# Kernel optimization log

Hardware: AMD Instinct MI355X
Metric: run time of the kernel (lower is better)

## Reference

```python
import jax, jax.numpy as jnp
import numpy as np
from functools import partial

B, T, F = 2048, 128, 64
H1, H2 = 512, 512


def _lstm(x, W, U, b, return_sequences):
    """Keras-semantics LSTM: gates order (i, f, c, o), recurrent_activation=sigmoid,
    cell activation=relu (as in activation='relu'). x: [B, T, F_in]."""
    Bs = x.shape[0]
    H = U.shape[0]
    # Precompute input contributions for all timesteps: [T, B, 4H]
    xg = (jnp.einsum('btf,fg->btg', x, W) + b).transpose(1, 0, 2)

    def step(carry, xt):
        h, c = carry
        g = xt + h @ U  # [B, 4H]
        i, f, cin, o = jnp.split(g, 4, axis=-1)
        i = jax.nn.sigmoid(i)
        f = jax.nn.sigmoid(f)
        o = jax.nn.sigmoid(o)
        c = f * c + i * jax.nn.relu(cin)
        h = o * jax.nn.relu(c)
        return (h, c), h

    h0 = jnp.zeros((Bs, H), dtype=x.dtype)
    c0 = jnp.zeros((Bs, H), dtype=x.dtype)
    (h, c), hs = jax.lax.scan(step, (h0, c0), xg)
    if return_sequences:
        return hs.transpose(1, 0, 2)  # [B, T, H]
    return h  # [B, H]


def setup_inputs() -> dict:
    key = jax.random.key(0)
    ks = jax.random.split(key, 9)
    s = 0.02  # small init so the relu cell stays numerically tame
    return {
        'x':  jax.random.normal(ks[0], (B, T, F), dtype=jnp.float32),
        'W1': jax.random.normal(ks[1], (F, 4 * H1), dtype=jnp.float32) * s,
        'U1': jax.random.normal(ks[2], (H1, 4 * H1), dtype=jnp.float32) * s,
        'b1': jnp.zeros((4 * H1,), dtype=jnp.float32),
        'W2': jax.random.normal(ks[3], (H1, 4 * H2), dtype=jnp.float32) * s,
        'U2': jax.random.normal(ks[4], (H2, 4 * H2), dtype=jnp.float32) * s,
        'b2': jnp.zeros((4 * H2,), dtype=jnp.float32),
        'Wd': jax.random.normal(ks[5], (H2, 1), dtype=jnp.float32) * s,
        'bd': jnp.zeros((1,), dtype=jnp.float32),
    }


def reference(x, W1, U1, b1, W2, U2, b2, Wd, bd):
    h1 = _lstm(x, W1, U1, b1, return_sequences=True)   # [B, T, H1]
    h2 = _lstm(h1, W2, U2, b2, return_sequences=False)  # [B, H2]
    return h2 @ Wd + bd  # [B, 1]
```

## Files before the change

### kernel.cpp

```cpp
#include <hip/hip_runtime.h>

#define TT   128
#define FF   64
#define HH   512
#define GG   2048
#define K1   576
#define K2   1024
#define KB1  72
#define KB2  128
#define NBLK 256
#define QS   520

using f16x8 = __attribute__((ext_vector_type(8))) _Float16;
using f16x4 = __attribute__((ext_vector_type(4))) _Float16;
using f32x4 = __attribute__((ext_vector_type(4))) float;

__global__ void pack_weights(const float* __restrict__ U, const float* __restrict__ W,
                             const float* __restrict__ bias, int K8, int Kh,
                             _Float16* __restrict__ Bp, float* __restrict__ pb)
{
    __shared__ _Float16 T[8][GG];
    const int kb = blockIdx.x;
    const int tid = threadIdx.x;
    for (int i = tid; i < 8 * (GG / 4); i += 256) {
        int r = i / (GG / 4), c4 = (i % (GG / 4)) * 4;
        int k = kb * 8 + r;
        const float* src = (k < Kh) ? (U + (size_t)k * GG) : (W + (size_t)(k - Kh) * GG);
        float4 v = *(const float4*)(src + c4);
        T[r][c4 + 0] = (_Float16)v.x; T[r][c4 + 1] = (_Float16)v.y;
        T[r][c4 + 2] = (_Float16)v.z; T[r][c4 + 3] = (_Float16)v.w;
    }
    __syncthreads();
    for (int m = tid; m < 2048; m += 256) {
        int ct = m >> 4, c = m & 15;
        int col = (c & 3) * HH + ct * 4 + (c >> 2);
        f16x8 v;
#pragma unroll
        for (int j = 0; j < 8; ++j) v[j] = T[j][col];
        *(f16x8*)(Bp + (((size_t)ct * K8 + kb) * 16 + c) * 8) = v;
    }
    if (kb == 0)
        for (int p = tid; p < GG; p += 256) {
            int ct = p >> 4, c = p & 15;
            pb[p] = bias[(c & 3) * HH + ct * 4 + (c >> 2)];
        }
}

template <int CTRL>
__device__ __forceinline__ float qbcast(float v) {
    return __int_as_float(__builtin_amdgcn_mov_dpp(__float_as_int(v), CTRL, 0xF, 0xF, true));
}

__device__ __forceinline__ void gld_lds16_sc0(const _Float16* g, _Float16* l) {
    __builtin_amdgcn_global_load_lds(
        (__attribute__((address_space(1))) const void*)g,
        (__attribute__((address_space(3))) void*)l, 16, 0, 1);
}

__device__ __forceinline__ void lstm_epi(
    f32x4 v4, float bias, float* __restrict__ cs, _Float16* __restrict__ hstp,
    int R0, int kq, int c, int ubase)
{
    const int gsel = c & 3;
    const int ub = ubase + (c >> 2);
#pragma unroll
    for (int j = 0; j < 4; ++j) {
        float v = v4[j] + bias;
        float sig = 1.f / (1.f + __expf(-v));
        float act = (gsel == 2) ? (v > 0.f ? v : 0.f) : sig;
        float ig  = qbcast<0x00>(act);
        float fg  = qbcast<0x55>(act);
        float cin = qbcast<0xAA>(act);
        float og  = qbcast<0xFF>(act);
        int Rl = kq * 4 + j;
        int R = R0 + Rl;
        float cp = cs[R * 33 + ub];
        float cn = fg * cp + ig * cin;
        float hn = og * (cn > 0.f ? cn : 0.f);
        if (gsel == 0) {
            cs[R * 33 + ub] = cn;
            hstp[Rl * 40 + ub] = (_Float16)hn;
        }
    }
}

#define MFMA16(av, bv, acc) \
    acc = __builtin_amdgcn_mfma_f32_16x16x32_f16(av, bv, acc, 0, 0, 0)

__global__ __launch_bounds__(256, 1) void lstm_persist(
    const float* __restrict__ x,
    const _Float16* __restrict__ Bp1, const float* __restrict__ pb1,
    const _Float16* __restrict__ Bp2, const float* __restrict__ pb2,
    const float* __restrict__ Wd, const float* __restrict__ bd,
    _Float16* __restrict__ h1b,
    _Float16* __restrict__ h2b,
    unsigned* __restrict__ bar,
    float* __restrict__ out)
{
    __shared__ _Float16 Q1[2][16 * QS];
    __shared__ _Float16 Q2[2][16 * QS];
    __shared__ _Float16 Xp[2][16][72];
    __shared__ float    c1s[128 * 33];
    __shared__ float    c2s[128 * 33];
    __shared__ _Float16 hst[2][2][16][40];
    __shared__ float    xb[2][2][2][2][2][256];

    const int tid = threadIdx.x;
    const int w = tid >> 6, lane = tid & 63;
    const int g = w >> 1, kh = w & 1;
    const int b = blockIdx.x;
    const int rg = 2 * (b & 7) + ((b >> 3) & 1);
    const int cg = b >> 4;
    const int r0 = rg * 128;
    const int c = lane & 15, kq = lane >> 4;

    for (int i = tid; i < 128 * 33; i += 256) { c1s[i] = 0.f; c2s[i] = 0.f; }

    f16x8 w1f[4][9], w2f[4][16];
#pragma unroll
    for (int ti = 0; ti < 4; ++ti) {
        const int ct = cg * 8 + g * 4 + ti;
#pragma unroll
        for (int kc = 0; kc < 9; ++kc)
            w1f[ti][kc] = *(const f16x8*)(Bp1 +
                (((size_t)ct * KB1 + (kh * 9 + kc) * 4 + kq) * 16 + c) * 8);
#pragma unroll
        for (int kc = 0; kc < 16; ++kc)
            w2f[ti][kc] = *(const f16x8*)(Bp2 +
                (((size_t)ct * KB2 + (kh * 16 + kc) * 4 + kq) * 16 + c) * 8);
    }
#pragma unroll
    for (int ti = 0; ti < 4; ++ti) {
#pragma unroll
        for (int kc = 0; kc < 9; ++kc) asm volatile("" : "+v"(w1f[ti][kc]));
#pragma unroll
        for (int kc = 0; kc < 16; ++kc) asm volatile("" : "+a"(w2f[ti][kc]));
    }

    const int ct0 = cg * 8 + g * 4 + kh * 2;
    const float bias1v[2] = { pb1[(ct0 + 0) * 16 + c], pb1[(ct0 + 1) * 16 + c] };
    const float bias2v[2] = { pb2[(ct0 + 0) * 16 + c], pb2[(ct0 + 1) * 16 + c] };
    const int ub0 = (g * 4 + kh * 2) * 4;

    const int xrow = tid >> 4, xc4 = (tid & 15) * 4;

    for (int s = 0; s <= TT; ++s) {
        const int pr1 = (s + 1) & 1, pw1 = s & 1;
        const int pr2 = s & 1,       pw2 = (s + 1) & 1;
        const _Float16* h1r = h1b + (size_t)pr1 * 2048 * HH;
        const _Float16* h2r = h2b + (size_t)pr2 * 2048 * HH;
        _Float16* h1w = h1b + (size_t)pw1 * 2048 * HH;
        _Float16* h2w = h2b + (size_t)pw2 * 2048 * HH;
        const bool notLast = (s < TT);

        {
#pragma unroll
            for (int i = 0; i < 4; ++i) {
                int r = w * 4 + i;
                gld_lds16_sc0(h1r + (size_t)(r0 + r) * HH + lane * 8, &Q1[0][r * QS]);
                gld_lds16_sc0(h2r + (size_t)(r0 + r) * HH + lane * 8, &Q2[0][r * QS]);
            }
            if (notLast) {
                float4 xv = *(const float4*)(x + ((size_t)(r0 + xrow) * TT + s) * FF + xc4);
                *(f16x4*)&Xp[0][xrow][xc4] =
                    (f16x4){(_Float16)xv.x, (_Float16)xv.y, (_Float16)xv.z, (_Float16)xv.w};
            }
        }
        __syncthreads();

        f32x4 ownA0{0.f, 0.f, 0.f, 0.f}, ownA1 = ownA0, ownB0 = ownA0, ownB1 = ownA0;

        for (int ch = 0; ch <= 9; ++ch) {
            const int par = ch & 1;

            if (ch <= 6) {
                const int gr = r0 + (ch + 1) * 16;
#pragma unroll
                for (int i = 0; i < 4; ++i) {
                    int r = w * 4 + i;
                    gld_lds16_sc0(h1r + (size_t)(gr + r) * HH + lane * 8, &Q1[par ^ 1][r * QS]);
                    gld_lds16_sc0(h2r + (size_t)(gr + r) * HH + lane * 8, &Q2[par ^ 1][r * QS]);
                }
            }
            float4 xnext{0.f, 0.f, 0.f, 0.f};
            const bool havex = (ch <= 6) && notLast;
            if (havex)
                xnext = *(const float4*)(x +
                    ((size_t)(r0 + (ch + 1) * 16 + xrow) * TT + s) * FF + xc4);

            if (ch >= 2) {
                int layer = tid >> 7, r = (tid >> 3) & 15, cq = tid & 7;
                bool go2 = layer ? (s >= 1) : notLast;
                if (go2) {
                    f16x4 hv = *(const f16x4*)&hst[par][layer][r][cq * 4];
                    _Float16* dst = (layer ? h2w : h1w)
                        + (size_t)(r0 + (ch - 2) * 16 + r) * HH + cg * 32 + cq * 4;
                    *(f16x4*)dst = hv;
                }
            }

            if (ch >= 1 && ch <= 8) {
                const int R0 = (ch - 1) * 16;
                if (notLast) {
                    f32x4 f0 = ownA0 + *(const f32x4*)&xb[par ^ 1][0][g][kh ^ 1][0][lane * 4];
                    f32x4 f1 = ownA1 + *(const f32x4*)&xb[par ^ 1][0][g][kh ^ 1][1][lane * 4];
                    lstm_epi(f0, bias1v[0], c1s, &hst[par ^ 1][0][0][0], R0, kq, c, ub0);
                    lstm_epi(f1, bias1v[1], c1s, &hst[par ^ 1][0][0][0], R0, kq, c, ub0 + 4);
                }
                if (s >= 1) {
                    f32x4 f0 = ownB0 + *(const f32x4*)&xb[par ^ 1][1][g][kh ^ 1][0][lane * 4];
                    f32x4 f1 = ownB1 + *(const f32x4*)&xb[par ^ 1][1][g][kh ^ 1][1][lane * 4];
                    lstm_epi(f0, bias2v[0], c2s, &hst[par ^ 1][1][0][0], R0, kq, c, ub0);
                    lstm_epi(f1, bias2v[1], c2s, &hst[par ^ 1][1][0][0], R0, kq, c, ub0 + 4);
                }
            }

            if (ch <= 7) {
                const char* q1b = (const char*)&Q1[par][0] + c * (QS * 2);
                const char* q2b = (const char*)&Q2[par][0] + c * (QS * 2);
                if (notLast) {
                    f32x4 a0{0.f, 0.f, 0.f, 0.f}, a1 = a0, a2 = a0, a3 = a0;
                    if (kh == 0) {
#pragma unroll
                        for (int kc = 0; kc < 9; ++kc) {
                            f16x8 av = *(const f16x8*)(q1b + kc * 64 + kq * 16);
                            MFMA16(av, w1f[0][kc], a0); MFMA16(av, w1f[1][kc], a1);
                            MFMA16(av, w1f[2][kc], a2); MFMA16(av, w1f[3][kc], a3);
                        }
                        *(f32x4*)&xb[par][0][g][0][0][lane * 4] = a2;
                        *(f32x4*)&xb[par][0][g][0][1][lane * 4] = a3;
                        ownA0 = a0; ownA1 = a1;
                    } else {
#pragma unroll
                        for (int kc = 0; kc < 7; ++kc) {
                            f16x8 av = *(const f16x8*)(q1b + (kc + 9) * 64 + kq * 16);
                            MFMA16(av, w1f[0][kc], a0); MFMA16(av, w1f[1][kc], a1);
                            MFMA16(av, w1f[2][kc], a2); MFMA16(av, w1f[3][kc], a3);
                        }
                        {
                            f16x8 av = *(const f16x8*)&Xp[par][c][kq * 8];
                            MFMA16(av, w1f[0][7], a0); MFMA16(av, w1f[1][7], a1);
                            MFMA16(av, w1f[2][7], a2); MFMA16(av, w1f[3][7], a3);
                        }
                        {
                            f16x8 av = *(const f16x8*)&Xp[par][c][32 + kq * 8];
                            MFMA16(av, w1f[0][8], a0); MFMA16(av, w1f[1][8], a1);
                            MFMA16(av, w1f[2][8], a2); MFMA16(av, w1f[3][8], a3);
                        }
                        *(f32x4*)&xb[par][0][g][1][0][lane * 4] = a0;
                        *(f32x4*)&xb[par][0][g][1][1][lane * 4] = a1;
                        ownA0 = a2; ownA1 = a3;
                    }
                }
                if (s >= 1) {
                    const char* qb = kh ? q1b : q2b;
                    f32x4 b0{0.f, 0.f, 0.f, 0.f}, b1 = b0, b2 = b0, b3 = b0;
#pragma unroll
                    for (int kc = 0; kc < 16; ++kc) {
                        f16x8 av = *(const f16x8*)(qb + kc * 64 + kq * 16);
                        MFMA16(av, w2f[0][kc], b0); MFMA16(av, w2f[1][kc], b1);
                        MFMA16(av, w2f[2][kc], b2); MFMA16(av, w2f[3][kc], b3);
                    }
                    if (kh == 0) {
                        *(f32x4*)&xb[par][1][g][0][0][lane * 4] = b2;
                        *(f32x4*)&xb[par][1][g][0][1][lane * 4] = b3;
                        ownB0 = b0; ownB1 = b1;
                    } else {
                        *(f32x4*)&xb[par][1][g][1][0][lane * 4] = b0;
                        *(f32x4*)&xb[par][1][g][1][1][lane * 4] = b1;
                        ownB0 = b2; ownB1 = b3;
                    }
                }
            }

            if (havex)
                *(f16x4*)&Xp[par ^ 1][xrow][xc4] =
                    (f16x4){(_Float16)xnext.x, (_Float16)xnext.y,
                            (_Float16)xnext.z, (_Float16)xnext.w};

            __syncthreads();
        }

        if (tid == 0) {
            __hip_atomic_fetch_add(&bar[rg * 32], 1u,
                                   __ATOMIC_RELAXED, __HIP_MEMORY_SCOPE_AGENT);
            const unsigned target = 16u * (unsigned)(s + 1);
            while (__hip_atomic_load(&bar[rg * 32],
                                     __ATOMIC_RELAXED, __HIP_MEMORY_SCOPE_AGENT) < target)
                __builtin_amdgcn_s_sleep(2);
        }
        __syncthreads();
    }

    if (cg == 0) {
        const _Float16* hf = h2b + (size_t)((TT + 1) & 1) * 2048 * HH;
        int row = tid >> 1, part = tid & 1;
        const _Float16* hr = hf + (size_t)(r0 + row) * HH + part * 256;
        const float* wd = Wd + part * 256;
        float ssum = 0.f;
#pragma unroll
        for (int u8 = 0; u8 < 32; ++u8) {
            f16x8 hv = *(const f16x8*)(hr + u8 * 8);
#pragma unroll
            for (int k = 0; k < 8; ++k) ssum += (float)hv[k] * wd[u8 * 8 + k];
        }
        ssum += __shfl_xor(ssum, 1);
        if (part == 0) out[r0 + row] = ssum + bd[0];
    }
}

extern "C" void kernel_launch(void* const* d_in, const int* in_sizes, int n_in,
                              void* d_out, int out_size, void* d_ws, size_t ws_size,
                              hipStream_t stream)
{
    const float* x  = (const float*)d_in[0];
    const float* W1 = (const float*)d_in[1];
    const float* U1 = (const float*)d_in[2];
    const float* b1 = (const float*)d_in[3];
    const float* W2 = (const float*)d_in[4];
    const float* U2 = (const float*)d_in[5];
    const float* b2 = (const float*)d_in[6];
    const float* Wd = (const float*)d_in[7];
    const float* bd = (const float*)d_in[8];
    float* out = (float*)d_out;

    char* ws = (char*)d_ws;
    size_t off = 0;
    _Float16* Bp1 = (_Float16*)(ws + off); off += (size_t)K1 * GG * 2;
    _Float16* Bp2 = (_Float16*)(ws + off); off += (size_t)K2 * GG * 2;
    float*    pb1 = (float*)(ws + off);    off += (size_t)GG * 4;
    float*    pb2 = (float*)(ws + off);    off += (size_t)GG * 4;
    _Float16* h1b = (_Float16*)(ws + off); off += (size_t)2 * 2048 * HH * 2;
    _Float16* h2b = (_Float16*)(ws + off); off += (size_t)2 * 2048 * HH * 2;
    unsigned* bar = (unsigned*)(ws + off); off += 16 * 32 * 4;

    hipMemsetAsync(h1b, 0, (size_t)2 * 2048 * HH * 2, stream);
    hipMemsetAsync(h2b, 0, (size_t)2 * 2048 * HH * 2, stream);
    hipMemsetAsync(bar, 0, 16 * 32 * 4, stream);

    pack_weights<<<KB1, 256, 0, stream>>>(U1, W1, b1, KB1, HH, Bp1, pb1);
    pack_weights<<<KB2, 256, 0, stream>>>(U2, W2, b2, KB2, HH, Bp2, pb2);
    lstm_persist<<<NBLK, 256, 0, stream>>>(x, Bp1, pb1, Bp2, pb2, Wd, bd,
                                           h1b, h2b, bar, out);
}
```

Before: 4.927 ms.

## Use 8 waves per block with one gate tile each, dropping cross-wave reduction

The persistent LSTM kernel moves from 4 waves (each holding 4 column tiles with a K-split across wave pairs) to 8 waves, each owning one 16-column tile over the full K range. This removes the LDS exchange buffer and its partial-sum reduction, and lets each wave run its own gate epilogue in the same chunk iteration, which shortens the chunk pipeline by one stage. Weights are pinned in AGPRs, per-thread load work is halved, and the final dense reduction uses 4 lanes per row. The risk is register pressure at 512 threads, and each wave now issues fewer independent MFMA chains per A-fragment load.

```diff
diff --git a/kernel.cpp b/kernel.cpp
--- a/kernel.cpp
+++ b/kernel.cpp
@@ -13,6 +13,7 @@
 
 using f16x8 = __attribute__((ext_vector_type(8))) _Float16;
 using f16x4 = __attribute__((ext_vector_type(4))) _Float16;
+using f16x2 = __attribute__((ext_vector_type(2))) _Float16;
 using f32x4 = __attribute__((ext_vector_type(4))) float;
 
 __global__ void pack_weights(const float* __restrict__ U, const float* __restrict__ W,
@@ -87,7 +88,7 @@
 #define MFMA16(av, bv, acc) \
     acc = __builtin_amdgcn_mfma_f32_16x16x32_f16(av, bv, acc, 0, 0, 0)
 
-__global__ __launch_bounds__(256, 1) void lstm_persist(
+__global__ __launch_bounds__(512, 2) void lstm_persist(
     const float* __restrict__ x,
     const _Float16* __restrict__ Bp1, const float* __restrict__ pb1,
     const _Float16* __restrict__ Bp2, const float* __restrict__ pb2,
@@ -103,46 +104,36 @@
     __shared__ float    c1s[128 * 33];
     __shared__ float    c2s[128 * 33];
     __shared__ _Float16 hst[2][2][16][40];
-    __shared__ float    xb[2][2][2][2][2][256];
 
     const int tid = threadIdx.x;
     const int w = tid >> 6, lane = tid & 63;
-    const int g = w >> 1, kh = w & 1;
     const int b = blockIdx.x;
     const int rg = 2 * (b & 7) + ((b >> 3) & 1);
     const int cg = b >> 4;
     const int r0 = rg * 128;
     const int c = lane & 15, kq = lane >> 4;
 
-    for (int i = tid; i < 128 * 33; i += 256) { c1s[i] = 0.f; c2s[i] = 0.f; }
-
-    f16x8 w1f[4][9], w2f[4][16];
-#pragma unroll
-    for (int ti = 0; ti < 4; ++ti) {
-        const int ct = cg * 8 + g * 4 + ti;
-#pragma unroll
-        for (int kc = 0; kc < 9; ++kc)
-            w1f[ti][kc] = *(const f16x8*)(Bp1 +
-                (((size_t)ct * KB1 + (kh * 9 + kc) * 4 + kq) * 16 + c) * 8);
-#pragma unroll
-        for (int kc = 0; kc < 16; ++kc)
-            w2f[ti][kc] = *(const f16x8*)(Bp2 +
-                (((size_t)ct * KB2 + (kh * 16 + kc) * 4 + kq) * 16 + c) * 8);
-    }
-#pragma unroll
-    for (int ti = 0; ti < 4; ++ti) {
-#pragma unroll
-        for (int kc = 0; kc < 9; ++kc) asm volatile("" : "+v"(w1f[ti][kc]));
-#pragma unroll
-        for (int kc = 0; kc < 16; ++kc) asm volatile("" : "+a"(w2f[ti][kc]));
-    }
-
-    const int ct0 = cg * 8 + g * 4 + kh * 2;
-    const float bias1v[2] = { pb1[(ct0 + 0) * 16 + c], pb1[(ct0 + 1) * 16 + c] };
-    const float bias2v[2] = { pb2[(ct0 + 0) * 16 + c], pb2[(ct0 + 1) * 16 + c] };
-    const int ub0 = (g * 4 + kh * 2) * 4;
-
-    const int xrow = tid >> 4, xc4 = (tid & 15) * 4;
+    for (int i = tid; i < 128 * 33; i += 512) { c1s[i] = 0.f; c2s[i] = 0.f; }
+    for (int i = tid; i < 2 * 2 * 16 * 40; i += 512) (&hst[0][0][0][0])[i] = (_Float16)0.f;
+
+    const int ct = cg * 8 + w;
+    f16x8 w1f[18], w2f[32];
+#pragma unroll
+    for (int kc = 0; kc < 18; ++kc)
+        w1f[kc] = *(const f16x8*)(Bp1 + (((size_t)ct * KB1 + kc * 4 + kq) * 16 + c) * 8);
+#pragma unroll
+    for (int kc = 0; kc < 32; ++kc)
+        w2f[kc] = *(const f16x8*)(Bp2 + (((size_t)ct * KB2 + kc * 4 + kq) * 16 + c) * 8);
+#pragma unroll
+    for (int kc = 0; kc < 18; ++kc) asm volatile("" : "+a"(w1f[kc]));
+#pragma unroll
+    for (int kc = 0; kc < 32; ++kc) asm volatile("" : "+a"(w2f[kc]));
+
+    const float bias1 = pb1[ct * 16 + c];
+    const float bias2 = pb2[ct * 16 + c];
+    const int ub0 = w * 4;
+
+    const int xrow = tid >> 5, xc2 = (tid & 31) * 2;
 
     for (int s = 0; s <= TT; ++s) {
         const int pr1 = (s + 1) & 1, pw1 = s & 1;
@@ -155,128 +146,86 @@
 
         {
 #pragma unroll
-            for (int i = 0; i < 4; ++i) {
-                int r = w * 4 + i;
+            for (int i = 0; i < 2; ++i) {
+                int r = w * 2 + i;
                 gld_lds16_sc0(h1r + (size_t)(r0 + r) * HH + lane * 8, &Q1[0][r * QS]);
                 gld_lds16_sc0(h2r + (size_t)(r0 + r) * HH + lane * 8, &Q2[0][r * QS]);
             }
             if (notLast) {
-                float4 xv = *(const float4*)(x + ((size_t)(r0 + xrow) * TT + s) * FF + xc4);
-                *(f16x4*)&Xp[0][xrow][xc4] =
-                    (f16x4){(_Float16)xv.x, (_Float16)xv.y, (_Float16)xv.z, (_Float16)xv.w};
+                float2 xv = *(const float2*)(x + ((size_t)(r0 + xrow) * TT + s) * FF + xc2);
+                *(f16x2*)&Xp[0][xrow][xc2] = (f16x2){(_Float16)xv.x, (_Float16)xv.y};
             }
         }
         __syncthreads();
 
-        f32x4 ownA0{0.f, 0.f, 0.f, 0.f}, ownA1 = ownA0, ownB0 = ownA0, ownB1 = ownA0;
-
-        for (int ch = 0; ch <= 9; ++ch) {
+        for (int ch = 0; ch <= 8; ++ch) {
             const int par = ch & 1;
 
             if (ch <= 6) {
                 const int gr = r0 + (ch + 1) * 16;
 #pragma unroll
-                for (int i = 0; i < 4; ++i) {
-                    int r = w * 4 + i;
+                for (int i = 0; i < 2; ++i) {
+                    int r = w * 2 + i;
                     gld_lds16_sc0(h1r + (size_t)(gr + r) * HH + lane * 8, &Q1[par ^ 1][r * QS]);
                     gld_lds16_sc0(h2r + (size_t)(gr + r) * HH + lane * 8, &Q2[par ^ 1][r * QS]);
                 }
             }
-            float4 xnext{0.f, 0.f, 0.f, 0.f};
+            float2 xnext{0.f, 0.f};
             const bool havex = (ch <= 6) && notLast;
             if (havex)
-                xnext = *(const float4*)(x +
-                    ((size_t)(r0 + (ch + 1) * 16 + xrow) * TT + s) * FF + xc4);
-
-            if (ch >= 2) {
+                xnext = *(const float2*)(x +
+                    ((size_t)(r0 + (ch + 1) * 16 + xrow) * TT + s) * FF + xc2);
+
+            if (ch >= 1 && tid < 256) {
                 int layer = tid >> 7, r = (tid >> 3) & 15, cq = tid & 7;
-                bool go2 = layer ? (s >= 1) : notLast;
-                if (go2) {
-                    f16x4 hv = *(const f16x4*)&hst[par][layer][r][cq * 4];
-                    _Float16* dst = (layer ? h2w : h1w)
-                        + (size_t)(r0 + (ch - 2) * 16 + r) * HH + cg * 32 + cq * 4;
-                    *(f16x4*)dst = hv;
-                }
-            }
-
-            if (ch >= 1 && ch <= 8) {
-                const int R0 = (ch - 1) * 16;
-                if (notLast) {
-                    f32x4 f0 = ownA0 + *(const f32x4*)&xb[par ^ 1][0][g][kh ^ 1][0][lane * 4];
-                    f32x4 f1 = ownA1 + *(const f32x4*)&xb[par ^ 1][0][g][kh ^ 1][1][lane * 4];
-                    lstm_epi(f0, bias1v[0], c1s, &hst[par ^ 1][0][0][0], R0, kq, c, ub0);
-                    lstm_epi(f1, bias1v[1], c1s, &hst[par ^ 1][0][0][0], R0, kq, c, ub0 + 4);
-                }
-                if (s >= 1) {
-                    f32x4 f0 = ownB0 + *(const f32x4*)&xb[par ^ 1][1][g][kh ^ 1][0][lane * 4];
-                    f32x4 f1 = ownB1 + *(const f32x4*)&xb[par ^ 1][1][g][kh ^ 1][1][lane * 4];
-                    lstm_epi(f0, bias2v[0], c2s, &hst[par ^ 1][1][0][0], R0, kq, c, ub0);
-                    lstm_epi(f1, bias2v[1], c2s, &hst[par ^ 1][1][0][0], R0, kq, c, ub0 + 4);
-                }
+                f16x4 hv = *(const f16x4*)&hst[par ^ 1][layer][r][cq * 4];
+                _Float16* dst = (layer ? h2w : h1w)
+                    + (size_t)(r0 + (ch - 1) * 16 + r) * HH + cg * 32 + cq * 4;
+                *(f16x4*)dst = hv;
             }
 
             if (ch <= 7) {
                 const char* q1b = (const char*)&Q1[par][0] + c * (QS * 2);
                 const char* q2b = (const char*)&Q2[par][0] + c * (QS * 2);
                 if (notLast) {
-                    f32x4 a0{0.f, 0.f, 0.f, 0.f}, a1 = a0, a2 = a0, a3 = a0;
-                    if (kh == 0) {
-#pragma unroll
-                        for (int kc = 0; kc < 9; ++kc) {
-                            f16x8 av = *(const f16x8*)(q1b + kc * 64 + kq * 16);
-                            MFMA16(av, w1f[0][kc], a0); MFMA16(av, w1f[1][kc], a1);
-                            MFMA16(av, w1f[2][kc], a2); MFMA16(av, w1f[3][kc], a3);
-                        }
-                        *(f32x4*)&xb[par][0][g][0][0][lane * 4] = a2;
-                        *(f32x4*)&xb[par][0][g][0][1][lane * 4] = a3;
-                        ownA0 = a0; ownA1 = a1;
-                    } else {
-#pragma unroll
-                        for (int kc = 0; kc < 7; ++kc) {
-                            f16x8 av = *(const f16x8*)(q1b + (kc + 9) * 64 + kq * 16);
-                            MFMA16(av, w1f[0][kc], a0); MFMA16(av, w1f[1][kc], a1);
-                            MFMA16(av, w1f[2][kc], a2); MFMA16(av, w1f[3][kc], a3);
-                        }
-                        {
-                            f16x8 av = *(const f16x8*)&Xp[par][c][kq * 8];
-                            MFMA16(av, w1f[0][7], a0); MFMA16(av, w1f[1][7], a1);
-                            MFMA16(av, w1f[2][7], a2); MFMA16(av, w1f[3][7], a3);
-                        }
-                        {
-                            f16x8 av = *(const f16x8*)&Xp[par][c][32 + kq * 8];
-                            MFMA16(av, w1f[0][8], a0); MFMA16(av, w1f[1][8], a1);
-                            MFMA16(av, w1f[2][8], a2); MFMA16(av, w1f[3][8], a3);
-                        }
-                        *(f32x4*)&xb[par][0][g][1][0][lane * 4] = a0;
-                        *(f32x4*)&xb[par][0][g][1][1][lane * 4] = a1;
-                        ownA0 = a2; ownA1 = a3;
-                    }
+                    f32x4 a0{0.f, 0.f, 0.f, 0.f}, a1 = a0;
+#pragma unroll
+                    for (int kc = 0; kc < 8; ++kc) {
+                        f16x8 av = *(const f16x8*)(q1b + kc * 64 + kq * 16);
+                        MFMA16(av, w1f[kc], a0);
+                    }
+#pragma unroll
+                    for (int kc = 8; kc < 16; ++kc) {
+                        f16x8 av = *(const f16x8*)(q1b + kc * 64 + kq * 16);
+                        MFMA16(av, w1f[kc], a1);
+                    }
+                    {
+                        f16x8 av = *(const f16x8*)&Xp[par][c][kq * 8];
+                        MFMA16(av, w1f[16], a0);
+                        av = *(const f16x8*)&Xp[par][c][32 + kq * 8];
+                        MFMA16(av, w1f[17], a1);
+                    }
+                    lstm_epi(a0 + a1, bias1, c1s, &hst[par][0][0][0], ch * 16, kq, c, ub0);
                 }
                 if (s >= 1) {
-                    const char* qb = kh ? q1b : q2b;
-                    f32x4 b0{0.f, 0.f, 0.f, 0.f}, b1 = b0, b2 = b0, b3 = b0;
+                    f32x4 b0{0.f, 0.f, 0.f, 0.f}, b1 = b0;
 #pragma unroll
                     for (int kc = 0; kc < 16; ++kc) {
-                        f16x8 av = *(const f16x8*)(qb + kc * 64 + kq * 16);
-                        MFMA16(av, w2f[0][kc], b0); MFMA16(av, w2f[1][kc], b1);
-                        MFMA16(av, w2f[2][kc], b2); MFMA16(av, w2f[3][kc], b3);
-                    }
-                    if (kh == 0) {
-                        *(f32x4*)&xb[par][1][g][0][0][lane * 4] = b2;
-                        *(f32x4*)&xb[par][1][g][0][1][lane * 4] = b3;
-                        ownB0 = b0; ownB1 = b1;
-                    } else {
-                        *(f32x4*)&xb[par][1][g][1][0][lane * 4] = b0;
-                        *(f32x4*)&xb[par][1][g][1][1][lane * 4] = b1;
-                        ownB0 = b2; ownB1 = b3;
-                    }
+                        f16x8 av = *(const f16x8*)(q2b + kc * 64 + kq * 16);
+                        MFMA16(av, w2f[kc], b0);
+                    }
+#pragma unroll
+                    for (int kc = 0; kc < 16; ++kc) {
+                        f16x8 av = *(const f16x8*)(q1b + kc * 64 + kq * 16);
+                        MFMA16(av, w2f[16 + kc], b1);
+                    }
+                    lstm_epi(b0 + b1, bias2, c2s, &hst[par][1][0][0], ch * 16, kq, c, ub0);
                 }
             }
 
             if (havex)
-                *(f16x4*)&Xp[par ^ 1][xrow][xc4] =
-                    (f16x4){(_Float16)xnext.x, (_Float16)xnext.y,
-                            (_Float16)xnext.z, (_Float16)xnext.w};
+                *(f16x2*)&Xp[par ^ 1][xrow][xc2] =
+                    (f16x2){(_Float16)xnext.x, (_Float16)xnext.y};
 
             __syncthreads();
         }
@@ -294,17 +243,18 @@
 
     if (cg == 0) {
         const _Float16* hf = h2b + (size_t)((TT + 1) & 1) * 2048 * HH;
-        int row = tid >> 1, part = tid & 1;
-        const _Float16* hr = hf + (size_t)(r0 + row) * HH + part * 256;
-        const float* wd = Wd + part * 256;
+        int row = tid >> 2, part = tid & 3;
+        const _Float16* hr = hf + (size_t)(r0 + row) * HH + part * 128;
+        const float* wd = Wd + part * 128;
         float ssum = 0.f;
 #pragma unroll
-        for (int u8 = 0; u8 < 32; ++u8) {
+        for (int u8 = 0; u8 < 16; ++u8) {
             f16x8 hv = *(const f16x8*)(hr + u8 * 8);
 #pragma unroll
             for (int k = 0; k < 8; ++k) ssum += (float)hv[k] * wd[u8 * 8 + k];
         }
         ssum += __shfl_xor(ssum, 1);
+        ssum += __shfl_xor(ssum, 2);
         if (part == 0) out[r0 + row] = ssum + bd[0];
     }
 }
@@ -340,6 +290,6 @@
 
     pack_weights<<<KB1, 256, 0, stream>>>(U1, W1, b1, KB1, HH, Bp1, pb1);
     pack_weights<<<KB2, 256, 0, stream>>>(U2, W2, b2, KB2, HH, Bp2, pb2);
-    lstm_persist<<<NBLK, 256, 0, stream>>>(x, Bp1, pb1, Bp2, pb2, Wd, bd,
+    lstm_persist<<<NBLK, 512, 0, stream>>>(x, Bp1, pb1, Bp2, pb2, Wd, bd,
                                            h1b, h2b, bar, out);
 }
```

Result: faster. 4.556 ms (-7.5%).
